# Kernel tuning notes

Hardware: AMD Instinct MI355X
Metric: run time of the kernel (lower is better)

## Reference

```python
import jax, jax.numpy as jnp
import numpy as np

Lenc = 2; Ldec = 2; H = 16
DE = 1024; DMLP = 4096; NV = 32000; LMAX = 2048
DATTN = 64; DMID = 64
BS = 4; LX = 512; LZ = 512
EPS = 1e-5
SCALE = 0.02


def setup_inputs() -> dict:
    key = jax.random.key(0)
    keys = iter(jax.random.split(key, 64))
    w = lambda shape: jax.random.normal(next(keys), shape, jnp.float32) * SCALE
    inp = {}
    inp['x'] = jax.random.randint(next(keys), (BS, LX), 0, NV)
    inp['z'] = jax.random.randint(next(keys), (BS, LZ), 0, NV)
    inp['We'] = w((NV, DE))
    inp['Wp'] = w((LMAX, DE))
    inp['Wu'] = w((NV, DE))
    for p, L, nln in (('enc', Lenc, 2), ('dec', Ldec, 3)):
        inp[p + '_Wq'] = w((L, H, DATTN, DE)); inp[p + '_bq'] = jnp.zeros((L, H, DATTN, 1))
        inp[p + '_Wk'] = w((L, H, DATTN, DE)); inp[p + '_bk'] = jnp.zeros((L, H, DATTN, 1))
        inp[p + '_Wv'] = w((L, H, DMID, DE)); inp[p + '_bv'] = jnp.zeros((L, H, DMID, 1))
        inp[p + '_Wo'] = w((L, DE, DMID * H)); inp[p + '_bo'] = jnp.zeros((L, DE, 1))
        inp[p + '_W1'] = w((L, DMLP, DE)); inp[p + '_b1'] = jnp.zeros((L, DMLP, 1))
        inp[p + '_W2'] = w((L, DE, DMLP)); inp[p + '_b2'] = jnp.zeros((L, DE, 1))
        for i in range(1, nln + 1):
            inp[f'{p}_ln{i}_g'] = jnp.ones((L, DE, 1))
            inp[f'{p}_ln{i}_b'] = jnp.zeros((L, DE, 1))
    return inp


def _ln(e, g, b):
    # normalize over feature dim (axis -2), torch unbiased variance (ddof=1)
    m = e.mean(axis=-2, keepdims=True)
    v = e.var(axis=-2, ddof=1, keepdims=True)
    return (e - m) / jnp.sqrt(v + EPS) * g + b


def _mha(X, Z, Wq, bq, Wk, bk, Wv, bv, Wo, bo, mask):
    # X: (b, de, lx); Z: (b, de, lz); per-head weights stacked on leading H axis
    q = jnp.einsum('had,bdl->bhal', Wq, X) + bq      # (b,H,dattn,lx)
    k = jnp.einsum('had,bdl->bhal', Wk, Z) + bk      # (b,H,dattn,lz)
    v = jnp.einsum('hod,bdl->bhol', Wv, Z) + bv      # (b,H,dmid,lz)
    score = jnp.einsum('bhak,bhaq->bhkq', k, q) / np.float32(np.sqrt(DATTN))  # (b,H,lz,lx)
    if mask is not None:
        score = jnp.where(mask == 0, -jnp.inf, score)
    attn = jax.nn.softmax(score, axis=-2)            # softmax over keys (dim -2), as in source
    Y = jnp.einsum('bhok,bhkq->bhoq', v, attn)       # (b,H,dmid,lx)
    Y = Y.reshape(Y.shape[0], H * DMID, Y.shape[-1]) # concat heads along feature dim
    return jnp.einsum('om,bml->bol', Wo, Y) + bo


def _mlp(E, W1, b1, W2, b2):
    h = jax.nn.relu(jnp.einsum('md,bdl->bml', W1, E) + b1)
    return jnp.einsum('dm,bml->bdl', W2, h) + b2


def _forward(We, Wp, Wu,
             enc_Wq, enc_bq, enc_Wk, enc_bk, enc_Wv, enc_bv, enc_Wo, enc_bo,
             enc_W1, enc_b1, enc_W2, enc_b2,
             enc_ln1_g, enc_ln1_b, enc_ln2_g, enc_ln2_b,
             dec_Wq, dec_bq, dec_Wk, dec_bk, dec_Wv, dec_bv, dec_Wo, dec_bo,
             dec_W1, dec_b1, dec_W2, dec_b2,
             dec_ln1_g, dec_ln1_b, dec_ln2_g, dec_ln2_b, dec_ln3_g, dec_ln3_b,
             x, z):
    lz = z.shape[-1]
    Z = We[z].swapaxes(-2, -1) + Wp[:lz].T           # (b, de, lz)
    for l in range(Lenc):
        Z = Z + _mha(Z, Z, enc_Wq[l], enc_bq[l], enc_Wk[l], enc_bk[l],
                     enc_Wv[l], enc_bv[l], enc_Wo[l], enc_bo[l], None)
        Z = _ln(Z, enc_ln1_g[l], enc_ln1_b[l])
        Z = Z + _mlp(Z, enc_W1[l], enc_b1[l], enc_W2[l], enc_b2[l])
        Z = _ln(Z, enc_ln2_g[l], enc_ln2_b[l])
    lx = x.shape[-1]
    X = We[x].swapaxes(-2, -1) + Wp[:lx].T           # (b, de, lx)
    causal = jnp.triu(jnp.ones((lx, lx), jnp.float32))  # mask[i,j]=1: key i can attend to query j (i<=j)
    for l in range(Ldec):
        # NOTE: source reuses the SAME attention weights for self- and cross-attention
        X = X + _mha(X, X, dec_Wq[l], dec_bq[l], dec_Wk[l], dec_bk[l],
                     dec_Wv[l], dec_bv[l], dec_Wo[l], dec_bo[l], causal)
        X = _ln(X, dec_ln1_g[l], dec_ln1_b[l])
        X = X + _mha(X, Z, dec_Wq[l], dec_bq[l], dec_Wk[l], dec_bk[l],
                     dec_Wv[l], dec_bv[l], dec_Wo[l], dec_bo[l], None)
        X = _ln(X, dec_ln2_g[l], dec_ln2_b[l])
        X = X + _mlp(X, dec_W1[l], dec_b1[l], dec_W2[l], dec_b2[l])
        X = _ln(X, dec_ln3_g[l], dec_ln3_b[l])
    return jax.nn.softmax(jnp.einsum('vd,bdl->bvl', Wu, X), axis=-2)  # (b, Nv, lx)


def reference(We, Wp, Wu,
              enc_Wq, enc_bq, enc_Wk, enc_bk, enc_Wv, enc_bv, enc_Wo, enc_bo,
              enc_W1, enc_b1, enc_W2, enc_b2,
              enc_ln1_g, enc_ln1_b, enc_ln2_g, enc_ln2_b,
              dec_Wq, dec_bq, dec_Wk, dec_bk, dec_Wv, dec_bv, dec_Wo, dec_bo,
              dec_W1, dec_b1, dec_W2, dec_b2,
              dec_ln1_g, dec_ln1_b, dec_ln2_g, dec_ln2_b, dec_ln3_g, dec_ln3_b,
              x, z):
    return _forward(We, Wp, Wu,
                    enc_Wq, enc_bq, enc_Wk, enc_bk, enc_Wv, enc_bv, enc_Wo, enc_bo,
                    enc_W1, enc_b1, enc_W2, enc_b2,
                    enc_ln1_g, enc_ln1_b, enc_ln2_g, enc_ln2_b,
                    dec_Wq, dec_bq, dec_Wk, dec_bk, dec_Wv, dec_bv, dec_Wo, dec_bo,
                    dec_W1, dec_b1, dec_W2, dec_b2,
                    dec_ln1_g, dec_ln1_b, dec_ln2_g, dec_ln2_b, dec_ln3_g, dec_ln3_b,
                    x, z)
```

## Files before the change

kernel.cpp:

```cpp
#include <hip/hip_runtime.h>
#include <hip/hip_bf16.h>
#include <math.h>

#define B_    4
#define LSEQ  512
#define DE    1024
#define NH    16
#define DA    64
#define DMLP  4096
#define NV    32000
#define TOK   (B_ * LSEQ)
#define EPSF  1e-5f

typedef __attribute__((ext_vector_type(8))) short bf16x8;
typedef __attribute__((ext_vector_type(4))) float f32x4;

static __device__ __forceinline__ void gl_lds16(const void* g, void* l) {
    __builtin_amdgcn_global_load_lds((const __attribute__((address_space(1))) void*)g,
                                     (__attribute__((address_space(3))) void*)l, 16, 0, 0);
}
static __device__ __forceinline__ float bf2f(unsigned short u) {
    return __uint_as_float(((unsigned)u) << 16);
}
static __device__ __forceinline__ unsigned short f2bf(float f) {
    union { __hip_bfloat16 h; unsigned short s; } u;
    u.h = __float2bfloat16(f);
    return u.s;
}

__global__ __launch_bounds__(256)
void convert_kernel(const float* __restrict__ src, unsigned short* __restrict__ dst)
{
    int i = (blockIdx.x * 256 + threadIdx.x) * 4;
    float4 v = *(const float4*)(src + i);
    ushort4 r;
    r.x = f2bf(v.x); r.y = f2bf(v.y); r.z = f2bf(v.z); r.w = f2bf(v.w);
    *(ushort4*)(dst + i) = r;
}

__global__ __launch_bounds__(256)
void pack_qkv_bias(const float* __restrict__ bq, const float* __restrict__ bk,
                   const float* __restrict__ bv, float* __restrict__ pb)
{
    int t = blockIdx.x * 256 + threadIdx.x;
    float v = (t < 1024) ? bq[t] : (t < 2048) ? bk[t - 1024] : bv[t - 2048];
    pb[t] = v;
}

__global__ __launch_bounds__(256)
void embed_kernel(const int* __restrict__ ids, const float* __restrict__ We,
                  const float* __restrict__ Wp, float* __restrict__ outf,
                  unsigned short* __restrict__ outb)
{
    int tk = blockIdx.x;
    int l  = tk & (LSEQ - 1);
    int idx = ids[tk];
    int d = threadIdx.x * 4;
    float4 a = *(const float4*)(We + (size_t)idx * DE + d);
    float4 b = *(const float4*)(Wp + (size_t)l * DE + d);
    float4 r; r.x = a.x + b.x; r.y = a.y + b.y; r.z = a.z + b.z; r.w = a.w + b.w;
    *(float4*)(outf + (size_t)tk * DE + d) = r;
    ushort4 rb; rb.x = f2bf(r.x); rb.y = f2bf(r.y); rb.z = f2bf(r.z); rb.w = f2bf(r.w);
    *(ushort4*)(outb + (size_t)tk * DE + d) = rb;
}

__global__ __launch_bounds__(256)
void gemm_bf16(const unsigned short* __restrict__ A, const unsigned short* __restrict__ W,
               const float* __restrict__ bias, const float* __restrict__ resid,
               float* __restrict__ Cf, unsigned short* __restrict__ Cb,
               int ldC, int K, int relu)
{
    __shared__ unsigned short Als[128 * 32];
    __shared__ unsigned short Wls[128 * 32];
    const int tid  = threadIdx.x;
    const int bm   = blockIdx.x << 7;
    const int bn   = blockIdx.y << 7;
    const int lane = tid & 63, wv = tid >> 6;
    const int wm   = (wv & 1) << 6, wn = (wv >> 1) << 6;
    const int fr   = lane & 15;
    const int fk   = (lane >> 4) << 3;
    const int cr   = (lane >> 4) << 2;

    const unsigned short* Ag = A + (size_t)(bm + (tid >> 2)) * K + ((tid & 3) << 3);
    const unsigned short* Wg = W + (size_t)(bn + (tid >> 2)) * K + ((tid & 3) << 3);
    unsigned short* Al0 = Als + (tid << 3);
    unsigned short* Wl0 = Wls + (tid << 3);

    f32x4 acc[4][4];
    #pragma unroll
    for (int i = 0; i < 4; ++i)
        #pragma unroll
        for (int j = 0; j < 4; ++j) acc[i][j] = (f32x4){0.f, 0.f, 0.f, 0.f};

    for (int k0 = 0; k0 < K; k0 += 32) {
        gl_lds16(Ag + k0,                 Al0);
        gl_lds16(Ag + (size_t)64 * K + k0, Al0 + 2048);
        gl_lds16(Wg + k0,                 Wl0);
        gl_lds16(Wg + (size_t)64 * K + k0, Wl0 + 2048);
        __syncthreads();
        bf16x8 af[4], wf[4];
        #pragma unroll
        for (int i = 0; i < 4; ++i) af[i] = *(const bf16x8*)&Als[(wm + i * 16 + fr) * 32 + fk];
        #pragma unroll
        for (int j = 0; j < 4; ++j) wf[j] = *(const bf16x8*)&Wls[(wn + j * 16 + fr) * 32 + fk];
        #pragma unroll
        for (int i = 0; i < 4; ++i)
            #pragma unroll
            for (int j = 0; j < 4; ++j)
                acc[i][j] = __builtin_amdgcn_mfma_f32_16x16x32_bf16(af[i], wf[j], acc[i][j], 0, 0, 0);
        __syncthreads();
    }

    #pragma unroll
    for (int i = 0; i < 4; ++i) {
        #pragma unroll
        for (int j = 0; j < 4; ++j) {
            const int n = bn + wn + j * 16 + fr;
            const float bs = bias ? bias[n] : 0.0f;
            #pragma unroll
            for (int r = 0; r < 4; ++r) {
                const int m = bm + wm + i * 16 + cr + r;
                float v = acc[i][j][r] + bs;
                if (resid) v += resid[(size_t)m * ldC + n];
                if (relu)  v = fmaxf(v, 0.0f);
                if (Cb) Cb[(size_t)m * ldC + n] = f2bf(v);
                else    Cf[(size_t)m * ldC + n] = v;
            }
        }
    }
}

__global__ __launch_bounds__(256)
void unembed_kernel(const float* __restrict__ Wu, const unsigned short* __restrict__ Xb,
                    float* __restrict__ out)
{
    __shared__ float          Als[128 * 32];
    __shared__ unsigned short Bls[128 * 32];
    const int tid  = threadIdx.x;
    const int bm   = blockIdx.y << 7;
    const int bn   = blockIdx.x << 7;
    const int lane = tid & 63, wv = tid >> 6;
    const int wm   = (wv & 1) << 6, wn = (wv >> 1) << 6;
    const int fr   = lane & 15;
    const int fk   = (lane >> 4) << 3;
    const int cr   = (lane >> 4) << 2;

    const float* Ag = Wu + (size_t)(bm + (tid >> 3)) * DE + ((tid & 7) << 2);
    const unsigned short* Bg = Xb + (size_t)(bn + (tid >> 2)) * DE + ((tid & 3) << 3);
    float* Al0 = Als + (tid << 2);
    unsigned short* Bl0 = Bls + (tid << 3);

    f32x4 acc[4][4];
    #pragma unroll
    for (int i = 0; i < 4; ++i)
        #pragma unroll
        for (int j = 0; j < 4; ++j) acc[i][j] = (f32x4){0.f, 0.f, 0.f, 0.f};

    for (int k0 = 0; k0 < DE; k0 += 32) {
        #pragma unroll
        for (int q = 0; q < 4; ++q)
            gl_lds16(Ag + (size_t)q * 32 * DE + k0, Al0 + q * 1024);
        gl_lds16(Bg + k0,                  Bl0);
        gl_lds16(Bg + (size_t)64 * DE + k0, Bl0 + 2048);
        __syncthreads();
        bf16x8 af[4], bf[4];
        #pragma unroll
        for (int i = 0; i < 4; ++i) {
            const float* ap = &Als[(wm + i * 16 + fr) * 32 + fk];
            f32x4 u0 = *(const f32x4*)ap;
            f32x4 u1 = *(const f32x4*)(ap + 4);
            bf16x8 t;
            t[0] = (short)f2bf(u0[0]); t[1] = (short)f2bf(u0[1]);
            t[2] = (short)f2bf(u0[2]); t[3] = (short)f2bf(u0[3]);
            t[4] = (short)f2bf(u1[0]); t[5] = (short)f2bf(u1[1]);
            t[6] = (short)f2bf(u1[2]); t[7] = (short)f2bf(u1[3]);
            af[i] = t;
        }
        #pragma unroll
        for (int j = 0; j < 4; ++j) bf[j] = *(const bf16x8*)&Bls[(wn + j * 16 + fr) * 32 + fk];
        #pragma unroll
        for (int i = 0; i < 4; ++i)
            #pragma unroll
            for (int j = 0; j < 4; ++j)
                acc[i][j] = __builtin_amdgcn_mfma_f32_16x16x32_bf16(af[i], bf[j], acc[i][j], 0, 0, 0);
        __syncthreads();
    }

    #pragma unroll
    for (int i = 0; i < 4; ++i) {
        #pragma unroll
        for (int j = 0; j < 4; ++j) {
            const int tok = bn + wn + j * 16 + fr;
            const int b2  = tok >> 9;
            const int lx  = tok & (LSEQ - 1);
            #pragma unroll
            for (int r = 0; r < 4; ++r) {
                const int v = bm + wm + i * 16 + cr + r;
                out[((size_t)b2 * NV + v) * LSEQ + lx] = acc[i][j][r];
            }
        }
    }
}

__global__ __launch_bounds__(256)
void attn_kernel(const unsigned short* __restrict__ QKV, unsigned short* __restrict__ Ctx,
                 int causal)
{
    __shared__ unsigned short Qls[128 * 64];
    __shared__ unsigned short Kls[128 * 64];
    __shared__ unsigned short Vt[64 * 136];
    __shared__ unsigned short Pq[128 * 136];
    __shared__ float redm[4][64];
    __shared__ float reds[4][64];
    __shared__ float scl[128];

    const int qt   = blockIdx.x;
    const int h    = blockIdx.y;
    const int b    = blockIdx.z;
    const int tid  = threadIdx.x;
    const int lane = tid & 63;
    const int wv   = tid >> 6;
    const int g    = lane >> 4;
    const int fr   = lane & 15;
    const int wm   = (wv & 1) << 6;
    const int wn   = (wv >> 1) << 6;
    const int q0   = qt << 7;

    const unsigned short* Qg = QKV + ((size_t)(b * LSEQ + q0)) * 3072 + h * 64;
    #pragma unroll
    for (int it = 0; it < 4; ++it) {
        const int ci = tid + it * 256;
        const int row = ci >> 3, c = (ci & 7) ^ (row & 7);
        gl_lds16(Qg + (size_t)row * 3072 + c * 8, Qls + ci * 8);
    }

    f32x4 acc_o[2][4];
    #pragma unroll
    for (int i = 0; i < 2; ++i)
        #pragma unroll
        for (int j = 0; j < 4; ++j) acc_o[i][j] = (f32x4){0.f, 0.f, 0.f, 0.f};
    float m_run[4], l_run[4];
    #pragma unroll
    for (int j = 0; j < 4; ++j) { m_run[j] = -INFINITY; l_run[j] = 0.0f; }

    const int ktmax = causal ? qt : 3;
    for (int kt = 0; kt <= ktmax; ++kt) {
        const int kz0 = kt << 7;
        __syncthreads();

        const unsigned short* Kg = QKV + ((size_t)(b * LSEQ + kz0)) * 3072 + 1024 + h * 64;
        #pragma unroll
        for (int it = 0; it < 4; ++it) {
            const int ci = tid + it * 256;
            const int row = ci >> 3, c = (ci & 7) ^ (row & 7);
            gl_lds16(Kg + (size_t)row * 3072 + c * 8, Kls + ci * 8);
        }
        bf16x8 v0[2], v1[2];
        const int kp = tid & 63;
        #pragma unroll
        for (int q2 = 0; q2 < 2; ++q2) {
            const int oc = (tid >> 6) + 4 * q2;
            const unsigned short* vg = QKV + ((size_t)(b * LSEQ + kz0 + 2 * kp)) * 3072
                                     + 2048 + h * 64 + oc * 8;
            v0[q2] = *(const bf16x8*)vg;
            v1[q2] = *(const bf16x8*)(vg + 3072);
        }
        #pragma unroll
        for (int q2 = 0; q2 < 2; ++q2) {
            const int oc = (tid >> 6) + 4 * q2;
            #pragma unroll
            for (int jj = 0; jj < 8; ++jj) {
                const unsigned int pk = (unsigned int)(unsigned short)v0[q2][jj]
                                      | ((unsigned int)(unsigned short)v1[q2][jj] << 16);
                *(unsigned int*)&Vt[(oc * 8 + jj) * 136 + 2 * kp] = pk;
            }
        }
        __syncthreads();

        f32x4 acc_s[4][4];
        #pragma unroll
        for (int i = 0; i < 4; ++i)
            #pragma unroll
            for (int j = 0; j < 4; ++j) acc_s[i][j] = (f32x4){0.f, 0.f, 0.f, 0.f};
        #pragma unroll
        for (int kc = 0; kc < 2; ++kc) {
            bf16x8 kf[4], qf[4];
            #pragma unroll
            for (int i = 0; i < 4; ++i) {
                const int row = wm + i * 16 + fr;
                kf[i] = *(const bf16x8*)(Kls + row * 64 + (((kc * 4 + g) ^ (row & 7)) << 3));
            }
            #pragma unroll
            for (int j = 0; j < 4; ++j) {
                const int row = wn + j * 16 + fr;
                qf[j] = *(const bf16x8*)(Qls + row * 64 + (((kc * 4 + g) ^ (row & 7)) << 3));
            }
            #pragma unroll
            for (int i = 0; i < 4; ++i)
                #pragma unroll
                for (int j = 0; j < 4; ++j)
                    acc_s[i][j] = __builtin_amdgcn_mfma_f32_16x16x32_bf16(kf[i], qf[j], acc_s[i][j], 0, 0, 0);
        }

        float tmax[4];
        #pragma unroll
        for (int j = 0; j < 4; ++j) tmax[j] = -INFINITY;
        #pragma unroll
        for (int i = 0; i < 4; ++i)
            #pragma unroll
            for (int j = 0; j < 4; ++j)
                #pragma unroll
                for (int r = 0; r < 4; ++r) {
                    float s = acc_s[i][j][r] * 0.125f;
                    if (causal) {
                        const int key = kz0 + wm + i * 16 + 4 * g + r;
                        const int qq  = q0 + wn + j * 16 + fr;
                        if (key > qq) s = -INFINITY;
                    }
                    acc_s[i][j][r] = s;
                    tmax[j] = fmaxf(tmax[j], s);
                }
        #pragma unroll
        for (int j = 0; j < 4; ++j) {
            float v = tmax[j];
            v = fmaxf(v, __shfl_xor(v, 16));
            v = fmaxf(v, __shfl_xor(v, 32));
            tmax[j] = v;
        }
        if (lane < 16)
            #pragma unroll
            for (int j = 0; j < 4; ++j) redm[wv][j * 16 + fr] = tmax[j];
        __syncthreads();
        float mnew[4], tsum[4];
        #pragma unroll
        for (int j = 0; j < 4; ++j) {
            tmax[j] = fmaxf(tmax[j], redm[wv ^ 1][j * 16 + fr]);
            mnew[j] = fmaxf(m_run[j], tmax[j]);
            tsum[j] = 0.0f;
        }
        #pragma unroll
        for (int i = 0; i < 4; ++i)
            #pragma unroll
            for (int j = 0; j < 4; ++j)
                #pragma unroll
                for (int r = 0; r < 4; ++r) {
                    const float p = __expf(acc_s[i][j][r] - mnew[j]);
                    acc_s[i][j][r] = p;
                    tsum[j] += p;
                }
        #pragma unroll
        for (int j = 0; j < 4; ++j) {
            float v = tsum[j];
            v += __shfl_xor(v, 16);
            v += __shfl_xor(v, 32);
            tsum[j] = v;
        }
        if (lane < 16)
            #pragma unroll
            for (int j = 0; j < 4; ++j) reds[wv][j * 16 + fr] = tsum[j];
        __syncthreads();
        float ef[4];
        #pragma unroll
        for (int j = 0; j < 4; ++j) {
            tsum[j] += reds[wv ^ 1][j * 16 + fr];
            ef[j] = __expf(m_run[j] - mnew[j]);
            l_run[j] = l_run[j] * ef[j] + tsum[j];
            m_run[j] = mnew[j];
        }
        if ((wv & 1) == 0 && lane < 16)
            #pragma unroll
            for (int j = 0; j < 4; ++j) scl[wn + j * 16 + fr] = ef[j];
        #pragma unroll
        for (int i = 0; i < 4; ++i)
            #pragma unroll
            for (int j = 0; j < 4; ++j) {
                short4 pk;
                pk.x = (short)f2bf(acc_s[i][j][0]);
                pk.y = (short)f2bf(acc_s[i][j][1]);
                pk.z = (short)f2bf(acc_s[i][j][2]);
                pk.w = (short)f2bf(acc_s[i][j][3]);
                *(short4*)&Pq[(wn + j * 16 + fr) * 136 + wm + i * 16 + 4 * g] = pk;
            }
        __syncthreads();

        float f0[2][4];
        #pragma unroll
        for (int i = 0; i < 2; ++i)
            #pragma unroll
            for (int r = 0; r < 4; ++r) f0[i][r] = scl[32 * wv + 16 * i + 4 * g + r];
        #pragma unroll
        for (int i = 0; i < 2; ++i)
            #pragma unroll
            for (int j = 0; j < 4; ++j)
                #pragma unroll
                for (int r = 0; r < 4; ++r) acc_o[i][j][r] *= f0[i][r];
        #pragma unroll
        for (int kc = 0; kc < 4; ++kc) {
            bf16x8 pa[2], vb[4];
            #pragma unroll
            for (int i = 0; i < 2; ++i)
                pa[i] = *(const bf16x8*)(Pq + (32 * wv + 16 * i + fr) * 136 + kc * 32 + 8 * g);
            #pragma unroll
            for (int j = 0; j < 4; ++j)
                vb[j] = *(const bf16x8*)(Vt + (16 * j + fr) * 136 + kc * 32 + 8 * g);
            #pragma unroll
            for (int i = 0; i < 2; ++i)
                #pragma unroll
                for (int j = 0; j < 4; ++j)
                    acc_o[i][j] = __builtin_amdgcn_mfma_f32_16x16x32_bf16(pa[i], vb[j], acc_o[i][j], 0, 0, 0);
        }
    }

    __syncthreads();
    if ((wv & 1) == 0 && lane < 16)
        #pragma unroll
        for (int j = 0; j < 4; ++j) scl[wn + j * 16 + fr] = 1.0f / l_run[j];
    __syncthreads();
    #pragma unroll
    for (int i = 0; i < 2; ++i) {
        #pragma unroll
        for (int r = 0; r < 4; ++r) {
            const int q  = q0 + 32 * wv + 16 * i + 4 * g + r;
            const float fl = scl[32 * wv + 16 * i + 4 * g + r];
            #pragma unroll
            for (int j = 0; j < 4; ++j) {
                const int d = 16 * j + fr;
                Ctx[((size_t)(b * LSEQ + q)) * DE + h * 64 + d] = f2bf(acc_o[i][j][r] * fl);
            }
        }
    }
}

__global__ __launch_bounds__(256)
void ln_kernel(const float* __restrict__ in, float* __restrict__ outf,
               unsigned short* __restrict__ outb,
               const float* __restrict__ g, const float* __restrict__ bb)
{
    __shared__ float red[256];
    const int tk  = blockIdx.x;
    const int tid = threadIdx.x;
    const float* xr = in + (size_t)tk * DE;
    const int d = tid * 4;
    float4 v = *(const float4*)(xr + d);

    red[tid] = v.x + v.y + v.z + v.w; __syncthreads();
    for (int st = 128; st > 0; st >>= 1) {
        if (tid < st) red[tid] += red[tid + st];
        __syncthreads();
    }
    const float mean = red[0] * (1.0f / DE);
    __syncthreads();

    float dx = v.x - mean, dy = v.y - mean, dz = v.z - mean, dw = v.w - mean;
    red[tid] = dx * dx + dy * dy + dz * dz + dw * dw;
    __syncthreads();
    for (int st = 128; st > 0; st >>= 1) {
        if (tid < st) red[tid] += red[tid + st];
        __syncthreads();
    }
    const float rstd = rsqrtf(red[0] * (1.0f / (DE - 1)) + EPSF);

    float4 gg = *(const float4*)(g + d);
    float4 b4 = *(const float4*)(bb + d);
    float4 r;
    r.x = dx * rstd * gg.x + b4.x;
    r.y = dy * rstd * gg.y + b4.y;
    r.z = dz * rstd * gg.z + b4.z;
    r.w = dw * rstd * gg.w + b4.w;
    *(float4*)(outf + (size_t)tk * DE + d) = r;
    ushort4 rb; rb.x = f2bf(r.x); rb.y = f2bf(r.y); rb.z = f2bf(r.z); rb.w = f2bf(r.w);
    *(ushort4*)(outb + (size_t)tk * DE + d) = rb;
}

#define VT1 50
__global__ __launch_bounds__(256)
void vsm_pass1(const float* __restrict__ out, float* __restrict__ Pm, float* __restrict__ Ps)
{
    __shared__ float sm[4][64], ss[4][64];
    const int tid = threadIdx.x, tx = tid & 63, ty = tid >> 6;
    const int l = blockIdx.x * 64 + tx, b = blockIdx.z, vt = blockIdx.y;
    const size_t base = ((size_t)b * NV + (size_t)vt * 640) * LSEQ + l;
    float m = -1e30f, s = 0.0f;
    for (int v = ty; v < 640; v += 4) {
        float w = out[base + (size_t)v * LSEQ];
        if (w > m) { s = s * __expf(m - w) + 1.0f; m = w; }
        else       { s += __expf(w - m); }
    }
    sm[ty][tx] = m; ss[ty][tx] = s;
    __syncthreads();
    if (ty == 0) {
        float M = sm[0][tx];
        #pragma unroll
        for (int q = 1; q < 4; ++q) M = fmaxf(M, sm[q][tx]);
        float S = 0.0f;
        #pragma unroll
        for (int q = 0; q < 4; ++q) S += ss[q][tx] * __expf(sm[q][tx] - M);
        const int tk = b * LSEQ + l;
        Pm[tk * VT1 + vt] = M;
        Ps[tk * VT1 + vt] = S;
    }
}

__global__ __launch_bounds__(256)
void vsm_pass2(const float* __restrict__ Pm, const float* __restrict__ Ps,
               float* __restrict__ Fm, float* __restrict__ Fr)
{
    const int tk = blockIdx.x * 256 + threadIdx.x;
    float M = -1e30f;
    for (int i = 0; i < VT1; ++i) M = fmaxf(M, Pm[tk * VT1 + i]);
    float S = 0.0f;
    for (int i = 0; i < VT1; ++i) S += Ps[tk * VT1 + i] * __expf(Pm[tk * VT1 + i] - M);
    Fm[tk] = M; Fr[tk] = 1.0f / S;
}

__global__ __launch_bounds__(256)
void vsm_pass3(float* __restrict__ out, const float* __restrict__ Fm, const float* __restrict__ Fr)
{
    const int tid = threadIdx.x, tx = tid & 63, ty = tid >> 6;
    const int l = blockIdx.x * 64 + tx, b = blockIdx.z;
    const int tk = b * LSEQ + l;
    const float M = Fm[tk], R = Fr[tk];
    const size_t base = ((size_t)b * NV + (size_t)blockIdx.y * 256) * LSEQ + l;
    for (int v = ty; v < 256; v += 4) {
        const size_t off = base + (size_t)v * LSEQ;
        out[off] = __expf(out[off] - M) * R;
    }
}

extern "C" void kernel_launch(void* const* d_in, const int* in_sizes, int n_in,
                              void* d_out, int out_size, void* d_ws, size_t ws_size,
                              hipStream_t stream)
{
    (void)in_sizes; (void)n_in; (void)out_size; (void)ws_size;
    const int*   x  = (const int*)d_in[0];
    const int*   z  = (const int*)d_in[1];
    const float* We = (const float*)d_in[2];
    const float* Wp = (const float*)d_in[3];
    const float* Wu = (const float*)d_in[4];
    const float* encW[12]; for (int i = 0; i < 12; ++i) encW[i] = (const float*)d_in[5 + i];
    const float* encLN[4]; for (int i = 0; i < 4;  ++i) encLN[i] = (const float*)d_in[17 + i];
    const float* decW[12]; for (int i = 0; i < 12; ++i) decW[i] = (const float*)d_in[21 + i];
    const float* decLN[6]; for (int i = 0; i < 6;  ++i) decLN[i] = (const float*)d_in[33 + i];
    float* out = (float*)d_out;

    const size_t MB = 1024 * 1024;
    char* w = (char*)d_ws;
    float* Z            = (float*)(w + 0 * MB);
    float* X            = (float*)(w + 8 * MB);
    float* T            = (float*)(w + 16 * MB);
    unsigned short* Zb  = (unsigned short*)(w + 24 * MB);
    unsigned short* Xb  = (unsigned short*)(w + 28 * MB);
    unsigned short* QKVb= (unsigned short*)(w + 32 * MB);
    unsigned short* Cxb = (unsigned short*)(w + 44 * MB);
    unsigned short* Hb  = (unsigned short*)(w + 48 * MB);
    unsigned short* Wqkvb = (unsigned short*)(w + 64 * MB);
    unsigned short* Wob   = (unsigned short*)(w + 70 * MB);
    unsigned short* W1b   = (unsigned short*)(w + 72 * MB);
    unsigned short* W2b   = (unsigned short*)(w + 80 * MB);
    float* pb = (float*)Hb;
    float* Pm = Z;
    float* Ps = Z + (size_t)TOK * VT1;
    float* Fm = Z + (size_t)TOK * 2 * VT1;
    float* Fr = Fm + TOK;

    auto conv = [&](const float* s, unsigned short* d, int n) {
        convert_kernel<<<n / 1024, 256, 0, stream>>>(s, d);
    };
    auto gemm = [&](const unsigned short* A, const unsigned short* Wt, const float* bias,
                    const float* resid, float* Cf, unsigned short* Cb, int ldC, int ntiles,
                    int K, int relu) {
        gemm_bf16<<<dim3(TOK / 128, ntiles), 256, 0, stream>>>(A, Wt, bias, resid, Cf, Cb,
                                                               ldC, K, relu);
    };
    auto lnorm = [&](const float* in, float* of, unsigned short* ob,
                     const float* g, const float* bb) {
        ln_kernel<<<TOK, 256, 0, stream>>>(in, of, ob, g, bb);
    };
    auto attn = [&](unsigned short* ctx, int causal) {
        attn_kernel<<<dim3(LSEQ / 128, NH, B_), 256, 0, stream>>>(QKVb, ctx, causal);
    };

    embed_kernel<<<TOK, 256, 0, stream>>>(z, We, Wp, Z, Zb);
    for (int l = 0; l < 2; ++l) {
        const size_t wo  = (size_t)l * DE * DE;
        const size_t bo  = (size_t)l * DE;
        const size_t w1o = (size_t)l * DMLP * DE;
        const size_t b1o = (size_t)l * DMLP;
        conv(encW[0] + wo, Wqkvb,                 DE * DE);
        conv(encW[2] + wo, Wqkvb + DE * DE,       DE * DE);
        conv(encW[4] + wo, Wqkvb + 2 * DE * DE,   DE * DE);
        pack_qkv_bias<<<12, 256, 0, stream>>>(encW[1] + bo, encW[3] + bo, encW[5] + bo, pb);
        gemm(Zb, Wqkvb, pb, nullptr, nullptr, QKVb, 3072, 24, DE, 0);
        attn(Cxb, 0);
        conv(encW[6] + wo, Wob, DE * DE);
        gemm(Cxb, Wob, encW[7] + bo, Z, T, nullptr, DE, 8, DE, 0);
        lnorm(T, Z, Zb, encLN[0] + bo, encLN[1] + bo);
        conv(encW[8] + w1o, W1b, DMLP * DE);
        gemm(Zb, W1b, encW[9] + b1o, nullptr, nullptr, Hb, DMLP, 32, DE, 1);
        conv(encW[10] + w1o, W2b, DMLP * DE);
        gemm(Hb, W2b, encW[11] + bo, Z, T, nullptr, DE, 8, DMLP, 0);
        lnorm(T, Z, Zb, encLN[2] + bo, encLN[3] + bo);
    }

    embed_kernel<<<TOK, 256, 0, stream>>>(x, We, Wp, X, Xb);
    for (int l = 0; l < 2; ++l) {
        const size_t wo  = (size_t)l * DE * DE;
        const size_t bo  = (size_t)l * DE;
        const size_t w1o = (size_t)l * DMLP * DE;
        const size_t b1o = (size_t)l * DMLP;
        conv(decW[0] + wo, Wqkvb,               DE * DE);
        conv(decW[2] + wo, Wqkvb + DE * DE,     DE * DE);
        conv(decW[4] + wo, Wqkvb + 2 * DE * DE, DE * DE);
        pack_qkv_bias<<<12, 256, 0, stream>>>(decW[1] + bo, decW[3] + bo, decW[5] + bo, pb);
        conv(decW[6] + wo, Wob, DE * DE);
        gemm(Xb, Wqkvb, pb, nullptr, nullptr, QKVb, 3072, 24, DE, 0);
        attn(Cxb, 1);
        gemm(Cxb, Wob, decW[7] + bo, X, T, nullptr, DE, 8, DE, 0);
        lnorm(T, X, Xb, decLN[0] + bo, decLN[1] + bo);
        gemm(Xb, Wqkvb, pb, nullptr, nullptr, QKVb, 3072, 8, DE, 0);
        gemm(Zb, Wqkvb + DE * DE, pb + 1024, nullptr, nullptr, QKVb + 1024, 3072, 16, DE, 0);
        attn(Cxb, 0);
        gemm(Cxb, Wob, decW[7] + bo, X, T, nullptr, DE, 8, DE, 0);
        lnorm(T, X, Xb, decLN[2] + bo, decLN[3] + bo);
        conv(decW[8] + w1o, W1b, DMLP * DE);
        gemm(Xb, W1b, decW[9] + b1o, nullptr, nullptr, Hb, DMLP, 32, DE, 1);
        conv(decW[10] + w1o, W2b, DMLP * DE);
        gemm(Hb, W2b, decW[11] + bo, X, T, nullptr, DE, 8, DMLP, 0);
        lnorm(T, X, Xb, decLN[4] + bo, decLN[5] + bo);
    }

    unembed_kernel<<<dim3(TOK / 128, NV / 128), 256, 0, stream>>>(Wu, Xb, out);
    vsm_pass1<<<dim3(LSEQ / 64, VT1, B_), 256, 0, stream>>>(out, Pm, Ps);
    vsm_pass2<<<TOK / 256, 256, 0, stream>>>(Pm, Ps, Fm, Fr);
    vsm_pass3<<<dim3(LSEQ / 64, NV / 256, B_), 256, 0, stream>>>(out, Fm, Fr);
}
```

Before: 2.327 ms.

## Fuse softmax partial stats into unembed, remap workgroups, merge QKV weight conversion

The softmax pass-1 reduction is folded into the unembed GEMM epilogue, which writes per-128-vocab-tile max and sum partials. This removes a full extra read of the 2000x32000 logits. The unembed A tile is now converted fp32→bf16 once while staging into a swizzled LDS layout, instead of every wave converting it after loading fp32 into LDS. Workgroup IDs in the GEMM, attention and unembed kernels are remapped (grouped by 8, likely intended to spread adjacent IDs across XCDs) for better cache locality, and the three QKV weight conversions are merged into one launch. In exchange, pass2 must reduce 250 partials per token instead of 50.

```diff
diff --git a/kernel.cpp b/kernel.cpp
--- a/kernel.cpp
+++ b/kernel.cpp
@@ -11,6 +11,7 @@
 #define NV    32000
 #define TOK   (B_ * LSEQ)
 #define EPSF  1e-5f
+#define NVT   250
 
 typedef __attribute__((ext_vector_type(8))) short bf16x8;
 typedef __attribute__((ext_vector_type(4))) float f32x4;
@@ -33,6 +34,18 @@
 {
     int i = (blockIdx.x * 256 + threadIdx.x) * 4;
     float4 v = *(const float4*)(src + i);
+    ushort4 r;
+    r.x = f2bf(v.x); r.y = f2bf(v.y); r.z = f2bf(v.z); r.w = f2bf(v.w);
+    *(ushort4*)(dst + i) = r;
+}
+
+__global__ __launch_bounds__(256)
+void convert3_kernel(const float* __restrict__ s0, const float* __restrict__ s1,
+                     const float* __restrict__ s2, unsigned short* __restrict__ dst)
+{
+    int i = (blockIdx.x * 256 + threadIdx.x) * 4;
+    const float* s = (i < DE * DE) ? s0 : (i < 2 * DE * DE) ? s1 : s2;
+    float4 v = *(const float4*)(s + (i & (DE * DE - 1)));
     ushort4 r;
     r.x = f2bf(v.x); r.y = f2bf(v.y); r.z = f2bf(v.z); r.w = f2bf(v.w);
     *(ushort4*)(dst + i) = r;
@@ -73,8 +86,11 @@
     __shared__ unsigned short Als[128 * 32];
     __shared__ unsigned short Wls[128 * 32];
     const int tid  = threadIdx.x;
-    const int bm   = blockIdx.x << 7;
-    const int bn   = blockIdx.y << 7;
+    const int nwg  = gridDim.y << 4;
+    const int lid  = (blockIdx.y << 4) + blockIdx.x;
+    const int wg   = (lid & 7) * (nwg >> 3) + (lid >> 3);
+    const int bm   = (wg & 15) << 7;
+    const int bn   = (wg >> 4) << 7;
     const int lane = tid & 63, wv = tid >> 6;
     const int wm   = (wv & 1) << 6, wn = (wv >> 1) << 6;
     const int fr   = lane & 15;
@@ -132,22 +148,32 @@
 
 __global__ __launch_bounds__(256)
 void unembed_kernel(const float* __restrict__ Wu, const unsigned short* __restrict__ Xb,
-                    float* __restrict__ out)
-{
-    __shared__ float          Als[128 * 32];
+                    float* __restrict__ out, float* __restrict__ Pm, float* __restrict__ Ps)
+{
+    __shared__ unsigned short Als[128 * 32];
     __shared__ unsigned short Bls[128 * 32];
+    __shared__ float redm[4][64], reds[4][64];
     const int tid  = threadIdx.x;
-    const int bm   = blockIdx.y << 7;
-    const int bn   = blockIdx.x << 7;
+    const int lid  = (blockIdx.y << 4) + blockIdx.x;
+    const int wg   = (lid & 7) * ((16 * NVT) >> 3) + (lid >> 3);
+    const int vt   = wg >> 4;
+    const int bm   = vt << 7;
+    const int bn   = (wg & 15) << 7;
     const int lane = tid & 63, wv = tid >> 6;
     const int wm   = (wv & 1) << 6, wn = (wv >> 1) << 6;
     const int fr   = lane & 15;
-    const int fk   = (lane >> 4) << 3;
-    const int cr   = (lane >> 4) << 2;
-
-    const float* Ag = Wu + (size_t)(bm + (tid >> 3)) * DE + ((tid & 7) << 2);
+    const int g    = lane >> 4;
+    const int fk   = g << 3;
+    const int cr   = g << 2;
+
+    const int srow = tid >> 1;
+    const int sch  = (tid & 1) << 1;
+    const float* Ag = Wu + (size_t)(bm + srow) * DE + (sch << 3);
+    const int sl0 = ((sch)     ^ ((srow >> 1) & 3)) << 3;
+    const int sl1 = ((sch + 1) ^ ((srow >> 1) & 3)) << 3;
+    unsigned short* Arow = Als + srow * 32;
+
     const unsigned short* Bg = Xb + (size_t)(bn + (tid >> 2)) * DE + ((tid & 3) << 3);
-    float* Al0 = Als + (tid << 2);
     unsigned short* Bl0 = Bls + (tid << 3);
 
     f32x4 acc[4][4];
@@ -157,32 +183,38 @@
         for (int j = 0; j < 4; ++j) acc[i][j] = (f32x4){0.f, 0.f, 0.f, 0.f};
 
     for (int k0 = 0; k0 < DE; k0 += 32) {
-        #pragma unroll
-        for (int q = 0; q < 4; ++q)
-            gl_lds16(Ag + (size_t)q * 32 * DE + k0, Al0 + q * 1024);
         gl_lds16(Bg + k0,                  Bl0);
         gl_lds16(Bg + (size_t)64 * DE + k0, Bl0 + 2048);
-        __syncthreads();
-        bf16x8 af[4], bf[4];
+        const float* ap = Ag + k0;
+        f32x4 u0 = *(const f32x4*)(ap);
+        f32x4 u1 = *(const f32x4*)(ap + 4);
+        f32x4 u2 = *(const f32x4*)(ap + 8);
+        f32x4 u3 = *(const f32x4*)(ap + 12);
+        bf16x8 t0, t1;
+        t0[0] = (short)f2bf(u0[0]); t0[1] = (short)f2bf(u0[1]);
+        t0[2] = (short)f2bf(u0[2]); t0[3] = (short)f2bf(u0[3]);
+        t0[4] = (short)f2bf(u1[0]); t0[5] = (short)f2bf(u1[1]);
+        t0[6] = (short)f2bf(u1[2]); t0[7] = (short)f2bf(u1[3]);
+        t1[0] = (short)f2bf(u2[0]); t1[1] = (short)f2bf(u2[1]);
+        t1[2] = (short)f2bf(u2[2]); t1[3] = (short)f2bf(u2[3]);
+        t1[4] = (short)f2bf(u3[0]); t1[5] = (short)f2bf(u3[1]);
+        t1[6] = (short)f2bf(u3[2]); t1[7] = (short)f2bf(u3[3]);
+        *(bf16x8*)(Arow + sl0) = t0;
+        *(bf16x8*)(Arow + sl1) = t1;
+        __syncthreads();
+        bf16x8 af[4], bfg[4];
         #pragma unroll
         for (int i = 0; i < 4; ++i) {
-            const float* ap = &Als[(wm + i * 16 + fr) * 32 + fk];
-            f32x4 u0 = *(const f32x4*)ap;
-            f32x4 u1 = *(const f32x4*)(ap + 4);
-            bf16x8 t;
-            t[0] = (short)f2bf(u0[0]); t[1] = (short)f2bf(u0[1]);
-            t[2] = (short)f2bf(u0[2]); t[3] = (short)f2bf(u0[3]);
-            t[4] = (short)f2bf(u1[0]); t[5] = (short)f2bf(u1[1]);
-            t[6] = (short)f2bf(u1[2]); t[7] = (short)f2bf(u1[3]);
-            af[i] = t;
-        }
-        #pragma unroll
-        for (int j = 0; j < 4; ++j) bf[j] = *(const bf16x8*)&Bls[(wn + j * 16 + fr) * 32 + fk];
+            const int row = wm + i * 16 + fr;
+            af[i] = *(const bf16x8*)&Als[row * 32 + ((g ^ ((row >> 1) & 3)) << 3)];
+        }
+        #pragma unroll
+        for (int j = 0; j < 4; ++j) bfg[j] = *(const bf16x8*)&Bls[(wn + j * 16 + fr) * 32 + fk];
         #pragma unroll
         for (int i = 0; i < 4; ++i)
             #pragma unroll
             for (int j = 0; j < 4; ++j)
-                acc[i][j] = __builtin_amdgcn_mfma_f32_16x16x32_bf16(af[i], bf[j], acc[i][j], 0, 0, 0);
+                acc[i][j] = __builtin_amdgcn_mfma_f32_16x16x32_bf16(af[i], bfg[j], acc[i][j], 0, 0, 0);
         __syncthreads();
     }
 
@@ -198,6 +230,44 @@
                 const int v = bm + wm + i * 16 + cr + r;
                 out[((size_t)b2 * NV + v) * LSEQ + lx] = acc[i][j][r];
             }
+        }
+    }
+
+    float pmx[4], psm[4];
+    #pragma unroll
+    for (int j = 0; j < 4; ++j) {
+        float m = acc[0][j][0];
+        #pragma unroll
+        for (int i = 0; i < 4; ++i)
+            #pragma unroll
+            for (int r = 0; r < 4; ++r) m = fmaxf(m, acc[i][j][r]);
+        m = fmaxf(m, __shfl_xor(m, 16));
+        m = fmaxf(m, __shfl_xor(m, 32));
+        pmx[j] = m;
+        float s = 0.0f;
+        #pragma unroll
+        for (int i = 0; i < 4; ++i)
+            #pragma unroll
+            for (int r = 0; r < 4; ++r) s += __expf(acc[i][j][r] - m);
+        s += __shfl_xor(s, 16);
+        s += __shfl_xor(s, 32);
+        psm[j] = s;
+    }
+    if (lane < 16) {
+        #pragma unroll
+        for (int j = 0; j < 4; ++j) { redm[wv][j * 16 + fr] = pmx[j]; reds[wv][j * 16 + fr] = psm[j]; }
+    }
+    __syncthreads();
+    if ((wv & 1) == 0 && lane < 16) {
+        #pragma unroll
+        for (int j = 0; j < 4; ++j) {
+            const float mo = redm[wv ^ 1][j * 16 + fr];
+            const float so = reds[wv ^ 1][j * 16 + fr];
+            const float M  = fmaxf(pmx[j], mo);
+            const float S  = psm[j] * __expf(pmx[j] - M) + so * __expf(mo - M);
+            const int tok  = bn + wn + j * 16 + fr;
+            Pm[(size_t)vt * TOK + tok] = M;
+            Ps[(size_t)vt * TOK + tok] = S;
         }
     }
 }
@@ -214,9 +284,11 @@
     __shared__ float reds[4][64];
     __shared__ float scl[128];
 
-    const int qt   = blockIdx.x;
-    const int h    = blockIdx.y;
-    const int b    = blockIdx.z;
+    const int lid = (blockIdx.z * 16 + blockIdx.y) * 4 + blockIdx.x;
+    const int wg  = (lid & 7) * 32 + (lid >> 3);
+    const int qt  = wg & 3;
+    const int h   = (wg >> 2) & 15;
+    const int b   = wg >> 6;
     const int tid  = threadIdx.x;
     const int lane = tid & 63;
     const int wv   = tid >> 6;
@@ -472,44 +544,15 @@
     *(ushort4*)(outb + (size_t)tk * DE + d) = rb;
 }
 
-#define VT1 50
-__global__ __launch_bounds__(256)
-void vsm_pass1(const float* __restrict__ out, float* __restrict__ Pm, float* __restrict__ Ps)
-{
-    __shared__ float sm[4][64], ss[4][64];
-    const int tid = threadIdx.x, tx = tid & 63, ty = tid >> 6;
-    const int l = blockIdx.x * 64 + tx, b = blockIdx.z, vt = blockIdx.y;
-    const size_t base = ((size_t)b * NV + (size_t)vt * 640) * LSEQ + l;
-    float m = -1e30f, s = 0.0f;
-    for (int v = ty; v < 640; v += 4) {
-        float w = out[base + (size_t)v * LSEQ];
-        if (w > m) { s = s * __expf(m - w) + 1.0f; m = w; }
-        else       { s += __expf(w - m); }
-    }
-    sm[ty][tx] = m; ss[ty][tx] = s;
-    __syncthreads();
-    if (ty == 0) {
-        float M = sm[0][tx];
-        #pragma unroll
-        for (int q = 1; q < 4; ++q) M = fmaxf(M, sm[q][tx]);
-        float S = 0.0f;
-        #pragma unroll
-        for (int q = 0; q < 4; ++q) S += ss[q][tx] * __expf(sm[q][tx] - M);
-        const int tk = b * LSEQ + l;
-        Pm[tk * VT1 + vt] = M;
-        Ps[tk * VT1 + vt] = S;
-    }
-}
-
 __global__ __launch_bounds__(256)
 void vsm_pass2(const float* __restrict__ Pm, const float* __restrict__ Ps,
                float* __restrict__ Fm, float* __restrict__ Fr)
 {
     const int tk = blockIdx.x * 256 + threadIdx.x;
     float M = -1e30f;
-    for (int i = 0; i < VT1; ++i) M = fmaxf(M, Pm[tk * VT1 + i]);
+    for (int i = 0; i < NVT; ++i) M = fmaxf(M, Pm[(size_t)i * TOK + tk]);
     float S = 0.0f;
-    for (int i = 0; i < VT1; ++i) S += Ps[tk * VT1 + i] * __expf(Pm[tk * VT1 + i] - M);
+    for (int i = 0; i < NVT; ++i) S += Ps[(size_t)i * TOK + tk] * __expf(Pm[(size_t)i * TOK + tk] - M);
     Fm[tk] = M; Fr[tk] = 1.0f / S;
 }
 
@@ -559,12 +602,15 @@
     unsigned short* W2b   = (unsigned short*)(w + 80 * MB);
     float* pb = (float*)Hb;
     float* Pm = Z;
-    float* Ps = Z + (size_t)TOK * VT1;
-    float* Fm = Z + (size_t)TOK * 2 * VT1;
+    float* Ps = Z + (size_t)NVT * TOK;
+    float* Fm = Z + (size_t)2 * NVT * TOK;
     float* Fr = Fm + TOK;
 
     auto conv = [&](const float* s, unsigned short* d, int n) {
         convert_kernel<<<n / 1024, 256, 0, stream>>>(s, d);
+    };
+    auto conv3 = [&](const float* s0, const float* s1, const float* s2, unsigned short* d) {
+        convert3_kernel<<<3 * DE * DE / 1024, 256, 0, stream>>>(s0, s1, s2, d);
     };
     auto gemm = [&](const unsigned short* A, const unsigned short* Wt, const float* bias,
                     const float* resid, float* Cf, unsigned short* Cb, int ldC, int ntiles,
@@ -586,9 +632,7 @@
         const size_t bo  = (size_t)l * DE;
         const size_t w1o = (size_t)l * DMLP * DE;
         const size_t b1o = (size_t)l * DMLP;
-        conv(encW[0] + wo, Wqkvb,                 DE * DE);
-        conv(encW[2] + wo, Wqkvb + DE * DE,       DE * DE);
-        conv(encW[4] + wo, Wqkvb + 2 * DE * DE,   DE * DE);
+        conv3(encW[0] + wo, encW[2] + wo, encW[4] + wo, Wqkvb);
         pack_qkv_bias<<<12, 256, 0, stream>>>(encW[1] + bo, encW[3] + bo, encW[5] + bo, pb);
         gemm(Zb, Wqkvb, pb, nullptr, nullptr, QKVb, 3072, 24, DE, 0);
         attn(Cxb, 0);
@@ -608,9 +652,7 @@
         const size_t bo  = (size_t)l * DE;
         const size_t w1o = (size_t)l * DMLP * DE;
         const size_t b1o = (size_t)l * DMLP;
-        conv(decW[0] + wo, Wqkvb,               DE * DE);
-        conv(decW[2] + wo, Wqkvb + DE * DE,     DE * DE);
-        conv(decW[4] + wo, Wqkvb + 2 * DE * DE, DE * DE);
+        conv3(decW[0] + wo, decW[2] + wo, decW[4] + wo, Wqkvb);
         pack_qkv_bias<<<12, 256, 0, stream>>>(decW[1] + bo, decW[3] + bo, decW[5] + bo, pb);
         conv(decW[6] + wo, Wob, DE * DE);
         gemm(Xb, Wqkvb, pb, nullptr, nullptr, QKVb, 3072, 24, DE, 0);
@@ -629,8 +671,7 @@
         lnorm(T, X, Xb, decLN[4] + bo, decLN[5] + bo);
     }
 
-    unembed_kernel<<<dim3(TOK / 128, NV / 128), 256, 0, stream>>>(Wu, Xb, out);
-    vsm_pass1<<<dim3(LSEQ / 64, VT1, B_), 256, 0, stream>>>(out, Pm, Ps);
+    unembed_kernel<<<dim3(TOK / 128, NVT), 256, 0, stream>>>(Wu, Xb, out, Pm, Ps);
     vsm_pass2<<<TOK / 256, 256, 0, stream>>>(Pm, Ps, Fm, Fr);
     vsm_pass3<<<dim3(LSEQ / 64, NV / 256, B_), 256, 0, stream>>>(out, Fm, Fr);
 }
```

After: 2.311 ms. No clear change (-0.7%).
